# Kernel tuning notes

Hardware: AMD Instinct MI355X
Metric: run time of the kernel (lower is better)

The kernel has to match this reference:

```python
import jax, jax.numpy as jnp
import numpy as np

IN_F = 4096
OUT_F = 4096
N = 16384


def setup_inputs() -> dict:
    key = jax.random.key(0)
    kx, kw = jax.random.split(key)
    x = jax.random.normal(kx, (N, IN_F), dtype=jnp.float32)
    # reset_parameters: weight ~ N(0, 1/in_features), bias = 0
    weight = jax.random.normal(kw, (OUT_F, IN_F), dtype=jnp.float32) * (1.0 / np.sqrt(IN_F))
    bias = jnp.zeros((OUT_F,), dtype=jnp.float32)
    return {"x": x, "weight": weight, "bias": bias}


def reference(x, weight, bias):
    # binary_linear_scalar: per-output-row scaling factor alpha = mean(|W|),
    # binarized weight bw = sign(W) * alpha  (XNOR-Net style)
    alpha = jnp.mean(jnp.abs(weight), axis=1, keepdims=True)  # [out, 1]
    bw = jnp.sign(weight) * alpha                             # [out, in]
    # y = x @ bw^T + bias
    return jnp.einsum('ni,oi->no', x, bw) + bias
```

## Files before the change

### kernel.cpp

```cpp
#include <hip/hip_runtime.h>
#include <hip/hip_bf16.h>
#include <stdint.h>

#define IN_F  4096
#define OUT_F 4096
#define NROWS 16384
#define NT    (IN_F / 64)

typedef unsigned short u16;
typedef __bf16 bf16x8 __attribute__((ext_vector_type(8)));
typedef float  f32x4  __attribute__((ext_vector_type(4)));
typedef u16    u16x8  __attribute__((ext_vector_type(8)));

#define BAR()   asm volatile("s_barrier" ::: "memory")
#define LGKM0() asm volatile("s_waitcnt lgkmcnt(0)" ::: "memory")
#define VM6()   asm volatile("s_waitcnt vmcnt(6)" ::: "memory")
#define VM0()   asm volatile("s_waitcnt vmcnt(0)" ::: "memory")

__device__ __forceinline__ u16 f2bf(float x) {
    union { float f; uint32_t u; } c; c.f = x;
    uint32_t u = c.u;
    return (u16)((u + 0x7FFFu + ((u >> 16) & 1u)) >> 16);
}

__device__ __forceinline__ void gload_lds16(const void* g, void* l) {
    __builtin_amdgcn_global_load_lds(
        (const __attribute__((address_space(1))) void*)g,
        (__attribute__((address_space(3))) void*)l, 16, 0, 0);
}

__device__ __forceinline__ u16 sgn_bf16(float v) {
    return v > 0.f ? 0x3F80 : (v < 0.f ? 0xBF80 : 0);
}

__global__ void prep_w_kernel(const float* __restrict__ W,
                              float* __restrict__ alpha,
                              u16* __restrict__ S, int swz) {
    const int row = blockIdx.x;
    const float* wr = W + (size_t)row * IN_F;
    float s = 0.f;
    for (int c = threadIdx.x; c < 512; c += 256) {
        const int g = c >> 3, c8 = c & 7;
        const int c8s = swz ? (c8 ^ (row & 7)) : c8;
        const f32x4* src = reinterpret_cast<const f32x4*>(wr + g * 64 + c8s * 8);
        f32x4 v0 = __builtin_nontemporal_load(src);
        f32x4 v1 = __builtin_nontemporal_load(src + 1);
        s += fabsf(v0[0]) + fabsf(v0[1]) + fabsf(v0[2]) + fabsf(v0[3])
           + fabsf(v1[0]) + fabsf(v1[1]) + fabsf(v1[2]) + fabsf(v1[3]);
        u16x8 r;
        r[0] = sgn_bf16(v0[0]); r[1] = sgn_bf16(v0[1]);
        r[2] = sgn_bf16(v0[2]); r[3] = sgn_bf16(v0[3]);
        r[4] = sgn_bf16(v1[0]); r[5] = sgn_bf16(v1[1]);
        r[6] = sgn_bf16(v1[2]); r[7] = sgn_bf16(v1[3]);
        *reinterpret_cast<u16x8*>(S + (size_t)row * IN_F + c * 8) = r;
    }
    for (int off = 32; off > 0; off >>= 1) s += __shfl_down(s, off);
    __shared__ float red[4];
    const int wave = threadIdx.x >> 6, lane = threadIdx.x & 63;
    if (lane == 0) red[wave] = s;
    __syncthreads();
    if (threadIdx.x == 0)
        alpha[row] = (red[0] + red[1] + red[2] + red[3]) * (1.0f / IN_F);
}

__global__ void convx_kernel(const float* __restrict__ X, u16* __restrict__ O,
                             int swz) {
    const size_t idx = (size_t)blockIdx.x * 256 + threadIdx.x;
    const int row = (int)(idx >> 9);
    const int q = (int)idx & 511;
    const int g = q >> 3, c8 = q & 7;
    const int c8s = swz ? (c8 ^ (row & 7)) : c8;
    const f32x4* src = reinterpret_cast<const f32x4*>(
        X + (size_t)row * IN_F + g * 64 + c8s * 8);
    f32x4 a = __builtin_nontemporal_load(src);
    f32x4 b = __builtin_nontemporal_load(src + 1);
    u16x8 r;
    r[0] = f2bf(a[0]); r[1] = f2bf(a[1]); r[2] = f2bf(a[2]); r[3] = f2bf(a[3]);
    r[4] = f2bf(b[0]); r[5] = f2bf(b[1]); r[6] = f2bf(b[2]); r[7] = f2bf(b[3]);
    reinterpret_cast<u16x8*>(O)[idx] = r;
}

__global__ __launch_bounds__(512, 2) void gemm8_kernel(
    const u16* __restrict__ Xbf, const u16* __restrict__ Wsign,
    const float* __restrict__ alpha, const float* __restrict__ bias,
    float* __restrict__ Y) {
    __shared__ u16 lds_[65536];

    const int tid  = threadIdx.x;
    const int lane = tid & 63, wave = tid >> 6;
    const int wm = wave >> 2, wn = wave & 3;
    const int lrow = lane & 15;

    const int wg = blockIdx.x;
    const int sz = ((wg & 7) << 7) | (wg >> 3);
    const int m0 = (sz & 63) * 256;
    const int n0 = (sz >> 6) * 256;

    const int q0 = (((lane >> 4) << 3)) ^ ((lrow & 7) << 3);
    const int q1 = q0 ^ 32;

    const u16* Ab0 = lds_ + (0 * 2 + wm) * 8192 + lrow * 64;
    const u16* Ab1 = lds_ + (1 * 2 + wm) * 8192 + lrow * 64;
    const u16* Bb0 = lds_ + 32768 + (0 * 2 + (wn >> 1)) * 8192 + ((wn & 1) * 64 + lrow) * 64;
    const u16* Bb1 = lds_ + 32768 + (1 * 2 + (wn >> 1)) * 8192 + ((wn & 1) * 64 + lrow) * 64;

    f32x4 acc[8][4];
#pragma unroll
    for (int i = 0; i < 8; ++i)
#pragma unroll
        for (int j = 0; j < 4; ++j) acc[i][j] = (f32x4){0.f, 0.f, 0.f, 0.f};

    auto stage = [&](int th, int j) {
        if (th >= NT) return;
        const u16* gb; int p0; u16* ls;
        if (j < 2) { gb = Wsign; p0 = n0 + j * 128;
                     ls = lds_ + 32768 + ((th & 1) * 2 + j) * 8192; }
        else       { gb = Xbf;   p0 = m0 + (j - 2) * 128;
                     ls = lds_ + ((th & 1) * 2 + (j - 2)) * 8192; }
#pragma unroll
        for (int t2 = 0; t2 < 2; ++t2) {
            const int c = t2 * 512 + tid;
            const int row = c >> 3, c8 = c & 7;
            gload_lds16(gb + (size_t)(p0 + row) * IN_F + th * 64 + c8 * 8,
                        ls + c * 8);
        }
    };

    auto ktile = [&](const u16* Abase, const u16* Bbase, int tau, bool last) {
        bf16x8 a0[4][2], a1[4][2], bfr[4][2];
#pragma unroll
        for (int mm = 0; mm < 4; ++mm) {
            a0[mm][0] = *reinterpret_cast<const bf16x8*>(Abase + mm * 1024 + q0);
            a0[mm][1] = *reinterpret_cast<const bf16x8*>(Abase + mm * 1024 + q1);
        }
#pragma unroll
        for (int nn = 0; nn < 4; ++nn) {
            bfr[nn][0] = *reinterpret_cast<const bf16x8*>(Bbase + nn * 1024 + q0);
            bfr[nn][1] = *reinterpret_cast<const bf16x8*>(Bbase + nn * 1024 + q1);
        }
        stage(tau + 1, 3);
        BAR(); LGKM0();
        __builtin_amdgcn_s_setprio(1);
#pragma unroll
        for (int mm = 0; mm < 4; ++mm)
#pragma unroll
            for (int nn = 0; nn < 2; ++nn) {
                acc[mm][nn] = __builtin_amdgcn_mfma_f32_16x16x32_bf16(a0[mm][0], bfr[nn][0], acc[mm][nn], 0, 0, 0);
                acc[mm][nn] = __builtin_amdgcn_mfma_f32_16x16x32_bf16(a0[mm][1], bfr[nn][1], acc[mm][nn], 0, 0, 0);
            }
        __builtin_amdgcn_s_setprio(0);
        BAR();
#pragma unroll
        for (int mm = 0; mm < 4; ++mm) {
            a1[mm][0] = *reinterpret_cast<const bf16x8*>(Abase + (4 + mm) * 1024 + q0);
            a1[mm][1] = *reinterpret_cast<const bf16x8*>(Abase + (4 + mm) * 1024 + q1);
        }
        stage(tau + 2, 0);
        BAR();
        __builtin_amdgcn_s_setprio(1);
#pragma unroll
        for (int mm = 0; mm < 4; ++mm)
#pragma unroll
            for (int nn = 0; nn < 2; ++nn) {
                acc[mm][2 + nn] = __builtin_amdgcn_mfma_f32_16x16x32_bf16(a0[mm][0], bfr[2 + nn][0], acc[mm][2 + nn], 0, 0, 0);
                acc[mm][2 + nn] = __builtin_amdgcn_mfma_f32_16x16x32_bf16(a0[mm][1], bfr[2 + nn][1], acc[mm][2 + nn], 0, 0, 0);
            }
        __builtin_amdgcn_s_setprio(0);
        BAR();
        stage(tau + 2, 1);
        BAR(); LGKM0();
        __builtin_amdgcn_s_setprio(1);
#pragma unroll
        for (int mm = 0; mm < 4; ++mm)
#pragma unroll
            for (int nn = 0; nn < 2; ++nn) {
                acc[4 + mm][nn] = __builtin_amdgcn_mfma_f32_16x16x32_bf16(a1[mm][0], bfr[nn][0], acc[4 + mm][nn], 0, 0, 0);
                acc[4 + mm][nn] = __builtin_amdgcn_mfma_f32_16x16x32_bf16(a1[mm][1], bfr[nn][1], acc[4 + mm][nn], 0, 0, 0);
            }
        __builtin_amdgcn_s_setprio(0);
        BAR();
        stage(tau + 2, 2);
        BAR();
        __builtin_amdgcn_s_setprio(1);
#pragma unroll
        for (int mm = 0; mm < 4; ++mm)
#pragma unroll
            for (int nn = 0; nn < 2; ++nn) {
                acc[4 + mm][2 + nn] = __builtin_amdgcn_mfma_f32_16x16x32_bf16(a1[mm][0], bfr[2 + nn][0], acc[4 + mm][2 + nn], 0, 0, 0);
                acc[4 + mm][2 + nn] = __builtin_amdgcn_mfma_f32_16x16x32_bf16(a1[mm][1], bfr[2 + nn][1], acc[4 + mm][2 + nn], 0, 0, 0);
            }
        __builtin_amdgcn_s_setprio(0);
        if (last) { VM0(); } else { VM6(); }
        BAR();
    };

    stage(0, 0); stage(0, 1); stage(0, 2); stage(0, 3);
    stage(1, 0); stage(1, 1); stage(1, 2);
    VM6();
    BAR();

    for (int it = 0; it < 32; ++it) {
        const bool last = (it == 31);
        ktile(Ab0, Bb0, 2 * it, last);
        ktile(Ab1, Bb1, 2 * it + 1, last);
    }

#pragma unroll
    for (int nf = 0; nf < 4; ++nf) {
        const int col = n0 + wn * 64 + nf * 16 + lrow;
        const float al = alpha[col], bi = bias[col];
#pragma unroll
        for (int mf = 0; mf < 8; ++mf) {
            const int rbase = m0 + wm * 128 + mf * 16 + ((lane >> 4) << 2);
#pragma unroll
            for (int r = 0; r < 4; ++r)
                __builtin_nontemporal_store(acc[mf][nf][r] * al + bi,
                    &Y[(size_t)(rbase + r) * OUT_F + col]);
        }
    }
}

__global__ __launch_bounds__(256) void gemm_fallback(
    const float* __restrict__ X, const u16* __restrict__ Wsign,
    const float* __restrict__ alpha, const float* __restrict__ bias,
    float* __restrict__ Y) {
    __shared__ u16 Alds[128 * 64];
    __shared__ u16 Blds[128 * 64];

    const int tid = threadIdx.x;
    const int n0 = blockIdx.x * 128;
    const int m0 = blockIdx.y * 128;
    const int wave = tid >> 6, lane = tid & 63;
    const int wm = wave >> 1, wn = wave & 1;
    const int lrow = lane & 15;
    const int lk8 = (lane >> 4) * 8;

    f32x4 acc[4][4];
#pragma unroll
    for (int i = 0; i < 4; ++i)
#pragma unroll
        for (int j = 0; j < 4; ++j) acc[i][j] = (f32x4){0.f, 0.f, 0.f, 0.f};

    for (int kt = 0; kt < IN_F; kt += 64) {
#pragma unroll
        for (int j = 0; j < 4; ++j) {
            const int idx = j * 256 + tid;
            const int row = idx >> 3, c8 = idx & 7;
            gload_lds16(Wsign + (size_t)(n0 + row) * IN_F + kt + c8 * 8,
                        &Blds[idx * 8]);
        }
#pragma unroll
        for (int j = 0; j < 4; ++j) {
            const int idx = j * 256 + tid;
            const int row = idx >> 3, c8 = idx & 7;
            const float* src = X + (size_t)(m0 + row) * IN_F + kt + c8 * 8;
            float4 v0 = *reinterpret_cast<const float4*>(src);
            float4 v1 = *reinterpret_cast<const float4*>(src + 4);
            u16x8 r;
            r[0] = f2bf(v0.x); r[1] = f2bf(v0.y); r[2] = f2bf(v0.z); r[3] = f2bf(v0.w);
            r[4] = f2bf(v1.x); r[5] = f2bf(v1.y); r[6] = f2bf(v1.z); r[7] = f2bf(v1.w);
            *reinterpret_cast<u16x8*>(&Alds[idx * 8]) = r;
        }
        __syncthreads();
#pragma unroll
        for (int kk = 0; kk < 2; ++kk) {
            bf16x8 af[4], bf[4];
#pragma unroll
            for (int mf = 0; mf < 4; ++mf)
                af[mf] = *reinterpret_cast<const bf16x8*>(
                    &Alds[(wm * 64 + mf * 16 + lrow) * 64 + kk * 32 + lk8]);
#pragma unroll
            for (int nf = 0; nf < 4; ++nf)
                bf[nf] = *reinterpret_cast<const bf16x8*>(
                    &Blds[(wn * 64 + nf * 16 + lrow) * 64 + kk * 32 + lk8]);
#pragma unroll
            for (int mf = 0; mf < 4; ++mf)
#pragma unroll
                for (int nf = 0; nf < 4; ++nf)
                    acc[mf][nf] = __builtin_amdgcn_mfma_f32_16x16x32_bf16(
                        af[mf], bf[nf], acc[mf][nf], 0, 0, 0);
        }
        __syncthreads();
    }
#pragma unroll
    for (int nf = 0; nf < 4; ++nf) {
        const int col = n0 + wn * 64 + nf * 16 + lrow;
        const float al = alpha[col], bi = bias[col];
#pragma unroll
        for (int mf = 0; mf < 4; ++mf) {
            const int rbase = m0 + wm * 64 + mf * 16 + (lane >> 4) * 4;
#pragma unroll
            for (int r = 0; r < 4; ++r)
                __builtin_nontemporal_store(acc[mf][nf][r] * al + bi,
                    &Y[(size_t)(rbase + r) * OUT_F + col]);
        }
    }
}

extern "C" void kernel_launch(void* const* d_in, const int* in_sizes, int n_in,
                              void* d_out, int out_size, void* d_ws, size_t ws_size,
                              hipStream_t stream) {
    const float* X    = (const float*)d_in[0];
    const float* W    = (const float*)d_in[1];
    const float* bias = (const float*)d_in[2];
    float* Y = (float*)d_out;

    char* ws = (char*)d_ws;
    float* alpha = (float*)ws;
    u16* Wsign   = (u16*)(ws + 16384);
    const size_t need_safe = 16384 + (size_t)OUT_F * IN_F * 2;
    const size_t need_fast = need_safe + (size_t)NROWS * IN_F * 2;

    if (ws_size >= need_fast) {
        u16* Xbf = (u16*)(ws + need_safe);
        prep_w_kernel<<<OUT_F, 256, 0, stream>>>(W, alpha, Wsign, 1);
        convx_kernel<<<(size_t)NROWS * IN_F / 8 / 256, 256, 0, stream>>>(X, Xbf, 1);
        gemm8_kernel<<<dim3(1024), 512, 0, stream>>>(Xbf, Wsign, alpha, bias, Y);
    } else {
        prep_w_kernel<<<OUT_F, 256, 0, stream>>>(W, alpha, Wsign, 0);
        dim3 grid(OUT_F / 128, NROWS / 128);
        gemm_fallback<<<grid, 256, 0, stream>>>(X, Wsign, alpha, bias, Y);
    }
}
```

Before: 620.5 us.

## Pack weight signs into bitmasks and expand to bf16 in registers

Weight signs are now packed one bit per element with a ballot-based prep kernel, giving a 64-bit word per 64 input columns. The GEMM reads these words straight from global memory into registers and expands them to ±1 bf16 fragments with bit selects, so only the activation tile goes through LDS. That LDS is now triple-buffered, the per-block LDS footprint shrinks, and the block-to-tile mapping changes. This cuts weight traffic and LDS staging at the cost of extra ALU work in the inner loop. Zero weights now map to -1 instead of 0, which only matters for exact zeros.

```diff
diff --git a/kernel.cpp b/kernel.cpp
--- a/kernel.cpp
+++ b/kernel.cpp
@@ -8,14 +8,14 @@
 #define NT    (IN_F / 64)
 
 typedef unsigned short u16;
+typedef unsigned long long u64;
 typedef __bf16 bf16x8 __attribute__((ext_vector_type(8)));
 typedef float  f32x4  __attribute__((ext_vector_type(4)));
 typedef u16    u16x8  __attribute__((ext_vector_type(8)));
 
 #define BAR()   asm volatile("s_barrier" ::: "memory")
 #define LGKM0() asm volatile("s_waitcnt lgkmcnt(0)" ::: "memory")
-#define VM6()   asm volatile("s_waitcnt vmcnt(6)" ::: "memory")
-#define VM0()   asm volatile("s_waitcnt vmcnt(0)" ::: "memory")
+#define VM4()   asm volatile("s_waitcnt vmcnt(4)" ::: "memory")
 
 __device__ __forceinline__ u16 f2bf(float x) {
     union { float f; uint32_t u; } c; c.f = x;
@@ -33,30 +33,23 @@
     return v > 0.f ? 0x3F80 : (v < 0.f ? 0xBF80 : 0);
 }
 
-__global__ void prep_w_kernel(const float* __restrict__ W,
-                              float* __restrict__ alpha,
-                              u16* __restrict__ S, int swz) {
+__global__ void prep_wbits_kernel(const float* __restrict__ W,
+                                  float* __restrict__ alpha,
+                                  u64* __restrict__ Wbits) {
     const int row = blockIdx.x;
+    const int wave = threadIdx.x >> 6, lane = threadIdx.x & 63;
     const float* wr = W + (size_t)row * IN_F;
     float s = 0.f;
-    for (int c = threadIdx.x; c < 512; c += 256) {
-        const int g = c >> 3, c8 = c & 7;
-        const int c8s = swz ? (c8 ^ (row & 7)) : c8;
-        const f32x4* src = reinterpret_cast<const f32x4*>(wr + g * 64 + c8s * 8);
-        f32x4 v0 = __builtin_nontemporal_load(src);
-        f32x4 v1 = __builtin_nontemporal_load(src + 1);
-        s += fabsf(v0[0]) + fabsf(v0[1]) + fabsf(v0[2]) + fabsf(v0[3])
-           + fabsf(v1[0]) + fabsf(v1[1]) + fabsf(v1[2]) + fabsf(v1[3]);
-        u16x8 r;
-        r[0] = sgn_bf16(v0[0]); r[1] = sgn_bf16(v0[1]);
-        r[2] = sgn_bf16(v0[2]); r[3] = sgn_bf16(v0[3]);
-        r[4] = sgn_bf16(v1[0]); r[5] = sgn_bf16(v1[1]);
-        r[6] = sgn_bf16(v1[2]); r[7] = sgn_bf16(v1[3]);
-        *reinterpret_cast<u16x8*>(S + (size_t)row * IN_F + c * 8) = r;
+#pragma unroll 4
+    for (int it = 0; it < 16; ++it) {
+        const int kword = it * 4 + wave;
+        float v = __builtin_nontemporal_load(wr + kword * 64 + lane);
+        s += fabsf(v);
+        u64 m = __ballot(v > 0.f);
+        if (lane == 0) Wbits[(size_t)row * 64 + kword] = m;
     }
     for (int off = 32; off > 0; off >>= 1) s += __shfl_down(s, off);
     __shared__ float red[4];
-    const int wave = threadIdx.x >> 6, lane = threadIdx.x & 63;
     if (lane == 0) red[wave] = s;
     __syncthreads();
     if (threadIdx.x == 0)
@@ -81,10 +74,10 @@
 }
 
 __global__ __launch_bounds__(512, 2) void gemm8_kernel(
-    const u16* __restrict__ Xbf, const u16* __restrict__ Wsign,
+    const u16* __restrict__ Xbf, const u64* __restrict__ Wbits,
     const float* __restrict__ alpha, const float* __restrict__ bias,
     float* __restrict__ Y) {
-    __shared__ u16 lds_[65536];
+    __shared__ u16 lds_[49152];
 
     const int tid  = threadIdx.x;
     const int lane = tid & 63, wave = tid >> 6;
@@ -92,53 +85,72 @@
     const int lrow = lane & 15;
 
     const int wg = blockIdx.x;
-    const int sz = ((wg & 7) << 7) | (wg >> 3);
-    const int m0 = (sz & 63) * 256;
-    const int n0 = (sz >> 6) * 256;
-
-    const int q0 = (((lane >> 4) << 3)) ^ ((lrow & 7) << 3);
+    const int i  = wg >> 3;
+    const int m0 = (((wg & 7) << 3) | (i >> 4)) << 8;
+    const int n0 = (i & 15) << 8;
+
+    const int q0 = ((lane >> 4) << 3) ^ ((lrow & 7) << 3);
     const int q1 = q0 ^ 32;
 
-    const u16* Ab0 = lds_ + (0 * 2 + wm) * 8192 + lrow * 64;
-    const u16* Ab1 = lds_ + (1 * 2 + wm) * 8192 + lrow * 64;
-    const u16* Bb0 = lds_ + 32768 + (0 * 2 + (wn >> 1)) * 8192 + ((wn & 1) * 64 + lrow) * 64;
-    const u16* Bb1 = lds_ + 32768 + (1 * 2 + (wn >> 1)) * 8192 + ((wn & 1) * 64 + lrow) * 64;
-
     f32x4 acc[8][4];
 #pragma unroll
-    for (int i = 0; i < 8; ++i)
-#pragma unroll
-        for (int j = 0; j < 4; ++j) acc[i][j] = (f32x4){0.f, 0.f, 0.f, 0.f};
-
-    auto stage = [&](int th, int j) {
+    for (int a = 0; a < 8; ++a)
+#pragma unroll
+        for (int b = 0; b < 4; ++b) acc[a][b] = (f32x4){0.f, 0.f, 0.f, 0.f};
+
+    auto stageA = [&](int th, int half, u16* buf) {
         if (th >= NT) return;
-        const u16* gb; int p0; u16* ls;
-        if (j < 2) { gb = Wsign; p0 = n0 + j * 128;
-                     ls = lds_ + 32768 + ((th & 1) * 2 + j) * 8192; }
-        else       { gb = Xbf;   p0 = m0 + (j - 2) * 128;
-                     ls = lds_ + ((th & 1) * 2 + (j - 2)) * 8192; }
 #pragma unroll
         for (int t2 = 0; t2 < 2; ++t2) {
-            const int c = t2 * 512 + tid;
+            const int c = half * 1024 + t2 * 512 + tid;
             const int row = c >> 3, c8 = c & 7;
-            gload_lds16(gb + (size_t)(p0 + row) * IN_F + th * 64 + c8 * 8,
-                        ls + c * 8);
+            gload_lds16(Xbf + (size_t)(m0 + row) * IN_F + th * 64 + c8 * 8,
+                        buf + c * 8);
         }
     };
 
-    auto ktile = [&](const u16* Abase, const u16* Bbase, int tau, bool last) {
+    u64 wcur[4], wnext[4];
+    auto loadB = [&](int th, u64* w) {
+        if (th >= NT) return;
+#pragma unroll
+        for (int nf = 0; nf < 4; ++nf)
+            w[nf] = Wbits[(size_t)(n0 + wn * 64 + nf * 16 + lrow) * 64 + th];
+    };
+
+    u16* b0 = lds_;
+    u16* b1 = lds_ + 16384;
+    u16* b2 = lds_ + 32768;
+
+    loadB(0, wcur);
+    stageA(0, 0, b0); stageA(0, 1, b0);
+    stageA(1, 0, b1); stageA(1, 1, b1);
+    VM4(); BAR();
+
+    u16* br = b0; u16* bn = b1; u16* bs = b2;
+    const int sh = (lane >> 4) << 3;
+
+    for (int t = 0; t < NT; ++t) {
+        const u16* Ab = br + wm * 8192 + lrow * 64;
         bf16x8 a0[4][2], a1[4][2], bfr[4][2];
+
 #pragma unroll
         for (int mm = 0; mm < 4; ++mm) {
-            a0[mm][0] = *reinterpret_cast<const bf16x8*>(Abase + mm * 1024 + q0);
-            a0[mm][1] = *reinterpret_cast<const bf16x8*>(Abase + mm * 1024 + q1);
-        }
-#pragma unroll
-        for (int nn = 0; nn < 4; ++nn) {
-            bfr[nn][0] = *reinterpret_cast<const bf16x8*>(Bbase + nn * 1024 + q0);
-            bfr[nn][1] = *reinterpret_cast<const bf16x8*>(Bbase + nn * 1024 + q1);
-        }
-        stage(tau + 1, 3);
+            a0[mm][0] = *reinterpret_cast<const bf16x8*>(Ab + mm * 1024 + q0);
+            a0[mm][1] = *reinterpret_cast<const bf16x8*>(Ab + mm * 1024 + q1);
+        }
+        loadB(t + 1, wnext);
+#pragma unroll
+        for (int nf = 0; nf < 4; ++nf)
+#pragma unroll
+            for (int kk = 0; kk < 2; ++kk) {
+                unsigned bb = (unsigned)(wcur[nf] >> (sh + kk * 32)) & 0xFFu;
+                union { unsigned u[4]; bf16x8 v; } r;
+#pragma unroll
+                for (int e = 0; e < 4; ++e)
+                    r.u[e] = (((bb >> (2 * e)) & 1u) ? 0x3F80u : 0xBF80u)
+                           | (((bb >> (2 * e + 1)) & 1u) ? 0x3F800000u : 0xBF800000u);
+                bfr[nf][kk] = r.v;
+            }
         BAR(); LGKM0();
         __builtin_amdgcn_s_setprio(1);
 #pragma unroll
@@ -150,12 +162,13 @@
             }
         __builtin_amdgcn_s_setprio(0);
         BAR();
+
 #pragma unroll
         for (int mm = 0; mm < 4; ++mm) {
-            a1[mm][0] = *reinterpret_cast<const bf16x8*>(Abase + (4 + mm) * 1024 + q0);
-            a1[mm][1] = *reinterpret_cast<const bf16x8*>(Abase + (4 + mm) * 1024 + q1);
-        }
-        stage(tau + 2, 0);
+            a1[mm][0] = *reinterpret_cast<const bf16x8*>(Ab + (4 + mm) * 1024 + q0);
+            a1[mm][1] = *reinterpret_cast<const bf16x8*>(Ab + (4 + mm) * 1024 + q1);
+        }
+        stageA(t + 2, 0, bs);
         BAR();
         __builtin_amdgcn_s_setprio(1);
 #pragma unroll
@@ -167,7 +180,8 @@
             }
         __builtin_amdgcn_s_setprio(0);
         BAR();
-        stage(tau + 2, 1);
+
+        stageA(t + 2, 1, bs);
         BAR(); LGKM0();
         __builtin_amdgcn_s_setprio(1);
 #pragma unroll
@@ -179,8 +193,7 @@
             }
         __builtin_amdgcn_s_setprio(0);
         BAR();
-        stage(tau + 2, 2);
-        BAR();
+
         __builtin_amdgcn_s_setprio(1);
 #pragma unroll
         for (int mm = 0; mm < 4; ++mm)
@@ -190,19 +203,11 @@
                 acc[4 + mm][2 + nn] = __builtin_amdgcn_mfma_f32_16x16x32_bf16(a1[mm][1], bfr[2 + nn][1], acc[4 + mm][2 + nn], 0, 0, 0);
             }
         __builtin_amdgcn_s_setprio(0);
-        if (last) { VM0(); } else { VM6(); }
-        BAR();
-    };
-
-    stage(0, 0); stage(0, 1); stage(0, 2); stage(0, 3);
-    stage(1, 0); stage(1, 1); stage(1, 2);
-    VM6();
-    BAR();
-
-    for (int it = 0; it < 32; ++it) {
-        const bool last = (it == 31);
-        ktile(Ab0, Bb0, 2 * it, last);
-        ktile(Ab1, Bb1, 2 * it + 1, last);
+        VM4(); BAR();
+
+        u16* tp = br; br = bn; bn = bs; bs = tp;
+#pragma unroll
+        for (int nf = 0; nf < 4; ++nf) wcur[nf] = wnext[nf];
     }
 
 #pragma unroll
@@ -218,6 +223,34 @@
                     &Y[(size_t)(rbase + r) * OUT_F + col]);
         }
     }
+}
+
+__global__ void prep_w_kernel(const float* __restrict__ W,
+                              float* __restrict__ alpha,
+                              u16* __restrict__ S) {
+    const int row = blockIdx.x;
+    const float* wr = W + (size_t)row * IN_F;
+    float s = 0.f;
+    for (int c = threadIdx.x; c < 512; c += 256) {
+        const f32x4* src = reinterpret_cast<const f32x4*>(wr + c * 8);
+        f32x4 v0 = __builtin_nontemporal_load(src);
+        f32x4 v1 = __builtin_nontemporal_load(src + 1);
+        s += fabsf(v0[0]) + fabsf(v0[1]) + fabsf(v0[2]) + fabsf(v0[3])
+           + fabsf(v1[0]) + fabsf(v1[1]) + fabsf(v1[2]) + fabsf(v1[3]);
+        u16x8 r;
+        r[0] = sgn_bf16(v0[0]); r[1] = sgn_bf16(v0[1]);
+        r[2] = sgn_bf16(v0[2]); r[3] = sgn_bf16(v0[3]);
+        r[4] = sgn_bf16(v1[0]); r[5] = sgn_bf16(v1[1]);
+        r[6] = sgn_bf16(v1[2]); r[7] = sgn_bf16(v1[3]);
+        *reinterpret_cast<u16x8*>(S + (size_t)row * IN_F + c * 8) = r;
+    }
+    for (int off = 32; off > 0; off >>= 1) s += __shfl_down(s, off);
+    __shared__ float red[4];
+    const int wave = threadIdx.x >> 6, lane = threadIdx.x & 63;
+    if (lane == 0) red[wave] = s;
+    __syncthreads();
+    if (threadIdx.x == 0)
+        alpha[row] = (red[0] + red[1] + red[2] + red[3]) * (1.0f / IN_F);
 }
 
 __global__ __launch_bounds__(256) void gemm_fallback(
@@ -237,9 +270,9 @@
 
     f32x4 acc[4][4];
 #pragma unroll
-    for (int i = 0; i < 4; ++i)
-#pragma unroll
-        for (int j = 0; j < 4; ++j) acc[i][j] = (f32x4){0.f, 0.f, 0.f, 0.f};
+    for (int a = 0; a < 4; ++a)
+#pragma unroll
+        for (int b = 0; b < 4; ++b) acc[a][b] = (f32x4){0.f, 0.f, 0.f, 0.f};
 
     for (int kt = 0; kt < IN_F; kt += 64) {
 #pragma unroll
@@ -264,21 +297,21 @@
         __syncthreads();
 #pragma unroll
         for (int kk = 0; kk < 2; ++kk) {
-            bf16x8 af[4], bf[4];
+            bf16x8 af[4], bfv[4];
 #pragma unroll
             for (int mf = 0; mf < 4; ++mf)
                 af[mf] = *reinterpret_cast<const bf16x8*>(
                     &Alds[(wm * 64 + mf * 16 + lrow) * 64 + kk * 32 + lk8]);
 #pragma unroll
             for (int nf = 0; nf < 4; ++nf)
-                bf[nf] = *reinterpret_cast<const bf16x8*>(
+                bfv[nf] = *reinterpret_cast<const bf16x8*>(
                     &Blds[(wn * 64 + nf * 16 + lrow) * 64 + kk * 32 + lk8]);
 #pragma unroll
             for (int mf = 0; mf < 4; ++mf)
 #pragma unroll
                 for (int nf = 0; nf < 4; ++nf)
                     acc[mf][nf] = __builtin_amdgcn_mfma_f32_16x16x32_bf16(
-                        af[mf], bf[nf], acc[mf][nf], 0, 0, 0);
+                        af[mf], bfv[nf], acc[mf][nf], 0, 0, 0);
         }
         __syncthreads();
     }
@@ -307,17 +340,20 @@
 
     char* ws = (char*)d_ws;
     float* alpha = (float*)ws;
-    u16* Wsign   = (u16*)(ws + 16384);
+    const size_t WBITS_OFF = 16384;
+    const size_t XBF_OFF   = WBITS_OFF + (size_t)OUT_F * (IN_F / 8);
+    const size_t need_fast = XBF_OFF + (size_t)NROWS * IN_F * 2;
     const size_t need_safe = 16384 + (size_t)OUT_F * IN_F * 2;
-    const size_t need_fast = need_safe + (size_t)NROWS * IN_F * 2;
 
     if (ws_size >= need_fast) {
-        u16* Xbf = (u16*)(ws + need_safe);
-        prep_w_kernel<<<OUT_F, 256, 0, stream>>>(W, alpha, Wsign, 1);
+        u64* Wbits = (u64*)(ws + WBITS_OFF);
+        u16* Xbf   = (u16*)(ws + XBF_OFF);
+        prep_wbits_kernel<<<OUT_F, 256, 0, stream>>>(W, alpha, Wbits);
         convx_kernel<<<(size_t)NROWS * IN_F / 8 / 256, 256, 0, stream>>>(X, Xbf, 1);
-        gemm8_kernel<<<dim3(1024), 512, 0, stream>>>(Xbf, Wsign, alpha, bias, Y);
+        gemm8_kernel<<<dim3(1024), 512, 0, stream>>>(Xbf, Wbits, alpha, bias, Y);
     } else {
-        prep_w_kernel<<<OUT_F, 256, 0, stream>>>(W, alpha, Wsign, 0);
+        u16* Wsign = (u16*)(ws + 16384);
+        prep_w_kernel<<<OUT_F, 256, 0, stream>>>(W, alpha, Wsign);
         dim3 grid(OUT_F / 128, NROWS / 128);
         gemm_fallback<<<grid, 256, 0, stream>>>(X, Wsign, alpha, bias, Y);
     }
```

New measurement: 733.4 us. 1.18x slower.
